# Kernel tuning notes

Hardware: AMD Instinct MI355X
Metric: run time of the kernel (lower is better)

## Reference

```python
import jax, jax.numpy as jnp
import numpy as np

B, S = 1, 2048
HID, NH, NKV, HD = 2048, 16, 4, 128
NREP = NH // NKV  # 4
WIN = 1024
ROPE_THETA = 10000.0


def rotate_half(t):
    t1, t2 = jnp.split(t, 2, axis=-1)
    return jnp.concatenate([-t2, t1], axis=-1)


def setup_inputs() -> dict:
    key = jax.random.key(0)
    ks = jax.random.split(key, 5)
    x = jax.random.normal(ks[0], (B, S, HID), dtype=jnp.float32)
    # causal sliding-window additive mask: 0 where attended, -1e9 elsewhere
    i = jnp.arange(S)
    allowed = (i[None, :] <= i[:, None]) & (i[:, None] - i[None, :] < WIN)
    attention_mask = jnp.where(allowed, 0.0, -1e9).astype(jnp.float32)[None, None]  # [1,1,S,S]
    wq = jax.random.normal(ks[1], (NH * HD, HID), dtype=jnp.float32) * 0.02
    wk = jax.random.normal(ks[2], (NKV * HD, HID), dtype=jnp.float32) * 0.02
    wv = jax.random.normal(ks[3], (NKV * HD, HID), dtype=jnp.float32) * 0.02
    wo = jax.random.normal(ks[4], (HID, NH * HD), dtype=jnp.float32) * 0.02
    return {"x": x, "attention_mask": attention_mask, "wq": wq, "wk": wk, "wv": wv, "wo": wo}


def reference(x, attention_mask, wq, wk, wv, wo):
    b, s, _ = x.shape
    q = (x @ wq.T).reshape(b, s, NH, HD)
    k = (x @ wk.T).reshape(b, s, NKV, HD)
    v = (x @ wv.T).reshape(b, s, NKV, HD)
    # rotary embeddings (HF-style rotate_half)
    inv_freq = 1.0 / (ROPE_THETA ** (jnp.arange(0, HD, 2, dtype=jnp.float32) / HD))
    freqs = jnp.arange(s, dtype=jnp.float32)[:, None] * inv_freq[None, :]  # [s, HD/2]
    emb = jnp.concatenate([freqs, freqs], axis=-1)  # [s, HD]
    cos = jnp.cos(emb)[None, :, None, :]
    sin = jnp.sin(emb)[None, :, None, :]
    q = q * cos + rotate_half(q) * sin
    k = k * cos + rotate_half(k) * sin
    # GQA: repeat kv heads
    k = jnp.repeat(k, NREP, axis=2)  # [b, s, NH, HD]
    v = jnp.repeat(v, NREP, axis=2)
    scores = jnp.einsum('bqhd,bkhd->bhqk', q, k) / jnp.sqrt(jnp.float32(HD)) + attention_mask
    probs = jax.nn.softmax(scores.astype(jnp.float32), axis=-1).astype(q.dtype)
    out = jnp.einsum('bhqk,bkhd->bqhd', probs, v).reshape(b, s, NH * HD)
    return out @ wo.T
```

## Files before the change

### kernel.cpp

```cpp
#include <hip/hip_runtime.h>


typedef short v8s __attribute__((ext_vector_type(8)));
typedef short v4s __attribute__((ext_vector_type(4)));
typedef float v4f __attribute__((ext_vector_type(4)));

__device__ __forceinline__ short f2bf(float f) {
  union { float f; unsigned u; } v; v.f = f;
  unsigned r = (v.u + 0x7FFFu + ((v.u >> 16) & 1u)) >> 16;
  return (short)r;
}
__device__ __forceinline__ float bf2f(short h) {
  union { unsigned u; float f; } v; v.u = ((unsigned)(unsigned short)h) << 16;
  return v.f;
}
__device__ __forceinline__ bool sniff_bf16(const unsigned* mask) {
  return mask[1] == 0xCE6ECE6Eu;
}

template <bool BF> struct Raw8;
template <> struct Raw8<true>  { v8s v; };
template <> struct Raw8<false> { float4 a, b; };

template <bool BF> __device__ __forceinline__ Raw8<BF> ldraw(const void* p, size_t e);
template <> __device__ __forceinline__ Raw8<true> ldraw<true>(const void* p, size_t e) {
  Raw8<true> r; r.v = *(const v8s*)((const short*)p + e); return r;
}
template <> __device__ __forceinline__ Raw8<false> ldraw<false>(const void* p, size_t e) {
  Raw8<false> r; const float* f = (const float*)p + e;
  r.a = *(const float4*)f; r.b = *(const float4*)(f + 4); return r;
}
template <bool BF> __device__ __forceinline__ v8s cvt8(const Raw8<BF>& r);
template <> __device__ __forceinline__ v8s cvt8<true>(const Raw8<true>& r) { return r.v; }
template <> __device__ __forceinline__ v8s cvt8<false>(const Raw8<false>& r) {
  v8s o;
  o[0] = f2bf(r.a.x); o[1] = f2bf(r.a.y); o[2] = f2bf(r.a.z); o[3] = f2bf(r.a.w);
  o[4] = f2bf(r.b.x); o[5] = f2bf(r.b.y); o[6] = f2bf(r.b.z); o[7] = f2bf(r.b.w);
  return o;
}

template <bool BFA, bool BFB>
__device__ __forceinline__ void gemm64x128_loop(
    const void* __restrict__ A, const void* __restrict__ Bt,
    int m0, int brow0, short* lA, short* lB, v4f acc[2][4])
{
  const int tid = threadIdx.x;
  const int w = tid >> 6, lane = tid & 63;
  const int quad = lane >> 4, r = lane & 15;
  const int wm = (w >> 1) * 32, wn = (w & 1) * 64;

  int uoffA[2]; size_t ea[2];
#pragma unroll
  for (int j = 0; j < 2; ++j) {
    int u = tid + 256 * j;
    int row = u >> 3, c = (u & 7) * 8;
    uoffA[j] = (c & 32) * 64 + row * 32 + (c & 31);
    ea[j] = (size_t)(m0 + row) * 2048 + c;
  }
  int uoffB[4]; size_t eb[4];
#pragma unroll
  for (int j = 0; j < 4; ++j) {
    int u = tid + 256 * j;
    int row = u >> 3, c = (u & 7) * 8;
    uoffB[j] = (c & 32) * 128 + row * 32 + (c & 31);
    eb[j] = (size_t)(brow0 + row) * 2048 + c;
  }

  for (int k0 = 0; k0 < 2048; k0 += 64) {
    Raw8<BFA> ta[2]; Raw8<BFB> tb[4];
#pragma unroll
    for (int j = 0; j < 2; ++j) ta[j] = ldraw<BFA>(A, ea[j] + k0);
#pragma unroll
    for (int j = 0; j < 4; ++j) tb[j] = ldraw<BFB>(Bt, eb[j] + k0);
    if (k0) __syncthreads();
#pragma unroll
    for (int j = 0; j < 2; ++j) *(v8s*)&lA[uoffA[j]] = cvt8<BFA>(ta[j]);
#pragma unroll
    for (int j = 0; j < 4; ++j) *(v8s*)&lB[uoffB[j]] = cvt8<BFB>(tb[j]);
    __syncthreads();
#pragma unroll
    for (int ks = 0; ks < 2; ++ks) {
      v8s a[2], b[4];
#pragma unroll
      for (int mt = 0; mt < 2; ++mt)
        a[mt] = *(const v8s*)&lA[ks * 2048 + (wm + mt * 16 + r) * 32 + quad * 8];
#pragma unroll
      for (int nt = 0; nt < 4; ++nt)
        b[nt] = *(const v8s*)&lB[ks * 4096 + (wn + nt * 16 + r) * 32 + quad * 8];
#pragma unroll
      for (int mt = 0; mt < 2; ++mt)
#pragma unroll
        for (int nt = 0; nt < 4; ++nt)
          acc[mt][nt] = __builtin_amdgcn_mfma_f32_16x16x32_bf16(a[mt], b[nt], acc[mt][nt], 0, 0, 0);
    }
  }
}

template <bool BF>
__device__ __forceinline__ void qkv_body(
    const void* X, const void* WQ, const void* WK, const void* WV,
    short* Qo, short* Ko, short* VTo)
{
  __shared__ __align__(16) short lA[64 * 64];
  __shared__ __align__(16) short lB[128 * 64];
  const int m0 = blockIdx.x * 64;
  const int n0 = blockIdx.y * 128;
  const void* Bt; int brow0;
  if (n0 < 2048)      { Bt = WQ; brow0 = n0; }
  else if (n0 < 2560) { Bt = WK; brow0 = n0 - 2048; }
  else                { Bt = WV; brow0 = n0 - 2560; }

  v4f acc[2][4];
#pragma unroll
  for (int i = 0; i < 2; ++i)
#pragma unroll
    for (int j = 0; j < 4; ++j) acc[i][j] = v4f{0.f, 0.f, 0.f, 0.f};

  gemm64x128_loop<BF, BF>(X, Bt, m0, brow0, lA, lB, acc);

  const int tid = threadIdx.x;
  const int w = tid >> 6, lane = tid & 63;
  const int quad = lane >> 4, r = lane & 15;
  const int wm = (w >> 1) * 32, wn = (w & 1) * 64;
  const int rowb = m0 + wm + quad * 4;

  if (n0 < 2048) {
#pragma unroll
    for (int mt = 0; mt < 2; ++mt)
#pragma unroll
      for (int nt = 0; nt < 4; ++nt) {
        int row = rowb + mt * 16;
        int col = n0 + wn + nt * 16 + r;
#pragma unroll
        for (int i = 0; i < 4; ++i)
          Qo[(size_t)(row + i) * 2048 + col] = f2bf(acc[mt][nt][i]);
      }
  } else if (n0 < 2560) {
#pragma unroll
    for (int mt = 0; mt < 2; ++mt)
#pragma unroll
      for (int nt = 0; nt < 4; ++nt) {
        int row = rowb + mt * 16;
        int col = n0 + wn + nt * 16 + r - 2048;
#pragma unroll
        for (int i = 0; i < 4; ++i)
          Ko[(size_t)(row + i) * 512 + col] = f2bf(acc[mt][nt][i]);
      }
  } else {
#pragma unroll
    for (int mt = 0; mt < 2; ++mt)
#pragma unroll
      for (int nt = 0; nt < 4; ++nt) {
        int row = rowb + mt * 16;
        int vcol = n0 + wn + nt * 16 + r - 2560;
        v4s pk;
#pragma unroll
        for (int i = 0; i < 4; ++i) pk[i] = f2bf(acc[mt][nt][i]);
        *(v4s*)&VTo[(size_t)vcol * 2048 + row] = pk;
      }
  }
}

__global__ __launch_bounds__(256, 3) void gemm_qkv(
    const void* __restrict__ X, const void* __restrict__ WQ,
    const void* __restrict__ WK, const void* __restrict__ WV,
    const unsigned* __restrict__ mask,
    short* __restrict__ Qo, short* __restrict__ Ko, short* __restrict__ VTo)
{
  if (sniff_bf16(mask)) qkv_body<true>(X, WQ, WK, WV, Qo, Ko, VTo);
  else                  qkv_body<false>(X, WQ, WK, WV, Qo, Ko, VTo);
}

__global__ __launch_bounds__(256) void rope_kernel(short* __restrict__ Q, short* __restrict__ K)
{
  const int t = blockIdx.x * 256 + threadIdx.x;
  const float L2T = 13.287712379549449f / 64.0f;
  int s, d; short* p; float scale;
  if (t < 2097152) {
    s = t >> 10; int rem = t & 1023; int h = rem >> 6; d = rem & 63;
    p = Q + (size_t)s * 2048 + h * 128 + d;
    scale = 0.08838834764831845f;
  } else {
    int u = t - 2097152;
    s = u >> 8; int rem = u & 255; int h = rem >> 6; d = rem & 63;
    p = K + (size_t)s * 512 + h * 128 + d;
    scale = 1.0f;
  }
  float inv = exp2f(-(float)d * L2T);
  float ang = (float)s * inv;
  float cs = cosf(ang), sn = sinf(ang);
  float x1 = bf2f(p[0]), x2 = bf2f(p[64]);
  p[0]  = f2bf((x1 * cs - x2 * sn) * scale);
  p[64] = f2bf((x2 * cs + x1 * sn) * scale);
}

__global__ __launch_bounds__(256, 1) void attn_kernel(
    const short* __restrict__ Q, const short* __restrict__ Kb,
    const short* __restrict__ VT, short* __restrict__ Ao)
{
  __shared__ __align__(16) short lK[64 * 128];
  __shared__ __align__(16) short lV[128 * 64];
  __shared__ __align__(16) short lP[4][16 * 72];

  const int bx = blockIdx.x;
  const int h = bx >> 5, qb = bx & 31;
  const int hk = h >> 2;
  const int q0 = qb * 64;
  const int tid = threadIdx.x, w = tid >> 6, lane = tid & 63;
  const int quad = lane >> 4, r = lane & 15;
  const int wq0 = q0 + w * 16;
  short* lPw = lP[w];

  v8s qa[4];
#pragma unroll
  for (int ks = 0; ks < 4; ++ks)
    qa[ks] = *(const v8s*)(Q + (size_t)(wq0 + r) * 2048 + h * 128 + ks * 32 + quad * 8);

  v4f Oa[8];
#pragma unroll
  for (int dt = 0; dt < 8; ++dt) Oa[dt] = v4f{0.f, 0.f, 0.f, 0.f};
  const float NEG = -3.0e38f;
  float m_i[4], l_i[4];
#pragma unroll
  for (int i = 0; i < 4; ++i) { m_i[i] = NEG; l_i[i] = 0.f; }

  const int t0 = (q0 >= 1024) ? ((q0 - 1023) >> 6) : 0;
  const int t1 = qb;

  for (int t = t0; t <= t1; ++t) {
    const int key0 = t << 6;
    v8s tK[4], tV[4];
#pragma unroll
    for (int u = 0; u < 4; ++u) {
      int lin = (w * 4 + u) * 64 + lane;
      int krow = lin >> 4, kcc = lin & 15;
      tK[u] = *(const v8s*)(Kb + (size_t)(key0 + krow) * 512 + hk * 128 + ((kcc ^ krow) & 15) * 8);
      int vrow = lin >> 3, vcc = lin & 7;
      tV[u] = *(const v8s*)(VT + (size_t)(hk * 128 + vrow) * 2048 + key0 + ((vcc ^ vrow) & 7) * 8);
    }
    if (t > t0) __syncthreads();
#pragma unroll
    for (int u = 0; u < 4; ++u) {
      int lin = (w * 4 + u) * 64 + lane;
      *(v8s*)&lK[lin * 8] = tK[u];
      *(v8s*)&lV[lin * 8] = tV[u];
    }
    __syncthreads();

    v4f s4[4];
#pragma unroll
    for (int nt = 0; nt < 4; ++nt) s4[nt] = v4f{0.f, 0.f, 0.f, 0.f};
#pragma unroll
    for (int ks = 0; ks < 4; ++ks)
#pragma unroll
      for (int nt = 0; nt < 4; ++nt) {
        v8s bk = *(const v8s*)&lK[(nt * 16 + r) * 128 + (((ks * 4 + quad) ^ r) & 15) * 8];
        s4[nt] = __builtin_amdgcn_mfma_f32_16x16x32_bf16(qa[ks], bk, s4[nt], 0, 0, 0);
      }

    float rowmax[4] = {NEG, NEG, NEG, NEG};
#pragma unroll
    for (int nt = 0; nt < 4; ++nt) {
      int key = key0 + nt * 16 + r;
#pragma unroll
      for (int i = 0; i < 4; ++i) {
        int q = wq0 + quad * 4 + i;
        bool ok = (key <= q) && (q - key < 1024);
        if (ok) rowmax[i] = fmaxf(rowmax[i], s4[nt][i]);
      }
    }
#pragma unroll
    for (int i = 0; i < 4; ++i)
#pragma unroll
      for (int off = 1; off < 16; off <<= 1)
        rowmax[i] = fmaxf(rowmax[i], __shfl_xor(rowmax[i], off, 64));
    float alpha[4], rsum[4] = {0.f, 0.f, 0.f, 0.f};
#pragma unroll
    for (int i = 0; i < 4; ++i) {
      float mn = fmaxf(m_i[i], rowmax[i]);
      alpha[i] = __expf(m_i[i] - mn);
      m_i[i] = mn;
    }
#pragma unroll
    for (int nt = 0; nt < 4; ++nt) {
      int key = key0 + nt * 16 + r;
#pragma unroll
      for (int i = 0; i < 4; ++i) {
        int q = wq0 + quad * 4 + i;
        bool ok = (key <= q) && (q - key < 1024);
        float p = ok ? __expf(s4[nt][i] - m_i[i]) : 0.0f;
        rsum[i] += p;
        lPw[(quad * 4 + i) * 72 + nt * 16 + r] = f2bf(p);
      }
    }
#pragma unroll
    for (int i = 0; i < 4; ++i) {
#pragma unroll
      for (int off = 1; off < 16; off <<= 1)
        rsum[i] += __shfl_xor(rsum[i], off, 64);
      l_i[i] = l_i[i] * alpha[i] + rsum[i];
    }
#pragma unroll
    for (int dt = 0; dt < 8; ++dt)
#pragma unroll
      for (int i = 0; i < 4; ++i) Oa[dt][i] *= alpha[i];

#pragma unroll
    for (int ks2 = 0; ks2 < 2; ++ks2) {
      v8s ap = *(const v8s*)&lPw[r * 72 + ks2 * 32 + quad * 8];
#pragma unroll
      for (int dt = 0; dt < 8; ++dt) {
        v8s bv = *(const v8s*)&lV[(dt * 16 + r) * 64 + (((ks2 * 4 + quad) ^ r) & 7) * 8];
        Oa[dt] = __builtin_amdgcn_mfma_f32_16x16x32_bf16(ap, bv, Oa[dt], 0, 0, 0);
      }
    }
  }

  float invl[4];
#pragma unroll
  for (int i = 0; i < 4; ++i) invl[i] = (l_i[i] > 0.f) ? 1.0f / l_i[i] : 0.f;
#pragma unroll
  for (int dt = 0; dt < 8; ++dt)
#pragma unroll
    for (int i = 0; i < 4; ++i) {
      int q = wq0 + quad * 4 + i;
      Ao[(size_t)q * 2048 + h * 128 + dt * 16 + r] = f2bf(Oa[dt][i] * invl[i]);
    }
}

template <bool BF>
__device__ __forceinline__ void out_body(
    const short* A, const void* WO, void* Out)
{
  __shared__ __align__(16) short lA[64 * 64];
  __shared__ __align__(16) short lB[128 * 64];
  const int m0 = blockIdx.x * 64;
  const int n0 = blockIdx.y * 128;

  v4f acc[2][4];
#pragma unroll
  for (int i = 0; i < 2; ++i)
#pragma unroll
    for (int j = 0; j < 4; ++j) acc[i][j] = v4f{0.f, 0.f, 0.f, 0.f};

  gemm64x128_loop<true, BF>(A, WO, m0, n0, lA, lB, acc);

  const int tid = threadIdx.x;
  const int w = tid >> 6, lane = tid & 63;
  const int quad = lane >> 4, r = lane & 15;
  const int wm = (w >> 1) * 32, wn = (w & 1) * 64;
  const int rowb = m0 + wm + quad * 4;
#pragma unroll
  for (int mt = 0; mt < 2; ++mt)
#pragma unroll
    for (int nt = 0; nt < 4; ++nt) {
      int row = rowb + mt * 16;
      int col = n0 + wn + nt * 16 + r;
#pragma unroll
      for (int i = 0; i < 4; ++i) {
        size_t idx = (size_t)(row + i) * 2048 + col;
        if (BF) ((short*)Out)[idx] = f2bf(acc[mt][nt][i]);
        else    ((float*)Out)[idx] = acc[mt][nt][i];
      }
    }
}

__global__ __launch_bounds__(256, 3) void gemm_out(
    const short* __restrict__ A, const void* __restrict__ WO,
    const unsigned* __restrict__ mask, void* __restrict__ Out)
{
  if (sniff_bf16(mask)) out_body<true>(A, WO, Out);
  else                  out_body<false>(A, WO, Out);
}

extern "C" void kernel_launch(void* const* d_in, const int* in_sizes, int n_in,
                              void* d_out, int out_size, void* d_ws, size_t ws_size,
                              hipStream_t stream) {
  const void*     x    = d_in[0];
  const unsigned* mask = (const unsigned*)d_in[1];
  const void*     wq   = d_in[2];
  const void*     wk   = d_in[3];
  const void*     wv   = d_in[4];
  const void*     wo   = d_in[5];

  short* Q  = (short*)d_out;
  short* Kb = (short*)d_ws;
  short* VT = Kb + (size_t)2048 * 512;
  short* Ao = VT + (size_t)2048 * 512;

  gemm_qkv<<<dim3(32, 24), 256, 0, stream>>>(x, wq, wk, wv, mask, Q, Kb, VT);
  rope_kernel<<<10240, 256, 0, stream>>>(Q, Kb);
  attn_kernel<<<512, 256, 0, stream>>>(Q, Kb, VT, Ao);
  gemm_out<<<dim3(32, 16), 256, 0, stream>>>(Ao, wo, mask, d_out);
}
```

Measured before the change: 259.1 us.

## Pre-convert inputs to bf16 and use direct global-to-LDS loads in GEMMs

Adds a conversion kernel that casts X and all weight matrices to bf16 in workspace once per call. The QKV and output GEMMs then load tiles with global_load_lds (direct DMA into LDS) rather than register-staged loads with per-element conversion. This is meant to cut per-tile fp32 conversion and register traffic in the GEMM inner loops. The cost is an extra pass over the weights every call plus more workspace, and the old path is kept as a fallback when the workspace is too small.

After: 229.9 us. 1.13x faster.

```diff
diff --git a/kernel.cpp b/kernel.cpp
--- a/kernel.cpp
+++ b/kernel.cpp
@@ -1,9 +1,16 @@
 #include <hip/hip_runtime.h>
 
+
+#define AS1 __attribute__((address_space(1)))
+#define AS3 __attribute__((address_space(3)))
 
 typedef short v8s __attribute__((ext_vector_type(8)));
 typedef short v4s __attribute__((ext_vector_type(4)));
 typedef float v4f __attribute__((ext_vector_type(4)));
+
+__device__ __forceinline__ void gload16(const void* g, void* l) {
+  __builtin_amdgcn_global_load_lds((AS1 void*)g, (AS3 void*)l, 16, 0, 0);
+}
 
 __device__ __forceinline__ short f2bf(float f) {
   union { float f; unsigned u; } v; v.f = f;
@@ -39,6 +46,178 @@
   return o;
 }
 
+__global__ __launch_bounds__(256) void convert_kernel(
+    const void* __restrict__ X, const void* __restrict__ WQ,
+    const void* __restrict__ WK, const void* __restrict__ WV,
+    const void* __restrict__ WO, const unsigned* __restrict__ mask,
+    short* __restrict__ Xbf, short* __restrict__ Wqkvbf, short* __restrict__ WObf)
+{
+  const bool bf = sniff_bf16(mask);
+  size_t e = ((size_t)blockIdx.x * 256 + threadIdx.x) * 8;
+  const void* src; short* dst; size_t off, doff;
+  if (e < 4194304)       { src = X;  dst = Xbf;  off = e; doff = e; }
+  else if (e < 10485760) {
+    size_t wv = e - 4194304; dst = Wqkvbf; doff = wv;
+    if (wv < 4194304)      { src = WQ; off = wv; }
+    else if (wv < 5242880) { src = WK; off = wv - 4194304; }
+    else                   { src = WV; off = wv - 5242880; }
+  }
+  else                   { src = WO; dst = WObf; off = e - 10485760; doff = off; }
+  v8s v = bf ? ldraw<true>(src, off).v : cvt8<false>(ldraw<false>(src, off));
+  *(v8s*)&dst[doff] = v;
+}
+
+__device__ __forceinline__ void gemm_dma_loop(
+    const short* __restrict__ A, const short* __restrict__ Bt,
+    int m0, int brow0, short* lA, short* lB, v4f acc[2][4])
+{
+  const int tid = threadIdx.x;
+  const int w = tid >> 6, lane = tid & 63;
+  const int quad = lane >> 4, r = lane & 15;
+  const int wm = (w >> 1) * 32, wn = (w & 1) * 64;
+  const int rlo = lane >> 2, c8 = (lane & 3) * 8;
+
+  size_t ga[2]; short* la[2];
+#pragma unroll
+  for (int j = 0; j < 2; ++j) {
+    int cA = w * 2 + j;
+    int p = cA >> 2, local = cA & 3;
+    ga[j] = (size_t)(m0 + local * 16 + rlo) * 2048 + p * 32 + c8;
+    la[j] = lA + cA * 512;
+  }
+  size_t gb[4]; short* lb[4];
+#pragma unroll
+  for (int j = 0; j < 4; ++j) {
+    int cB = w * 4 + j;
+    int p = cB >> 3, local = cB & 7;
+    gb[j] = (size_t)(brow0 + local * 16 + rlo) * 2048 + p * 32 + c8;
+    lb[j] = lB + cB * 512;
+  }
+
+  for (int k0 = 0; k0 < 2048; k0 += 64) {
+    if (k0) __syncthreads();
+#pragma unroll
+    for (int j = 0; j < 2; ++j) gload16(A + ga[j] + k0, la[j]);
+#pragma unroll
+    for (int j = 0; j < 4; ++j) gload16(Bt + gb[j] + k0, lb[j]);
+    __syncthreads();
+#pragma unroll
+    for (int ks = 0; ks < 2; ++ks) {
+      v8s a[2], b[4];
+#pragma unroll
+      for (int mt = 0; mt < 2; ++mt)
+        a[mt] = *(const v8s*)&lA[ks * 2048 + (wm + mt * 16 + r) * 32 + quad * 8];
+#pragma unroll
+      for (int nt = 0; nt < 4; ++nt)
+        b[nt] = *(const v8s*)&lB[ks * 4096 + (wn + nt * 16 + r) * 32 + quad * 8];
+#pragma unroll
+      for (int mt = 0; mt < 2; ++mt)
+#pragma unroll
+        for (int nt = 0; nt < 4; ++nt)
+          acc[mt][nt] = __builtin_amdgcn_mfma_f32_16x16x32_bf16(a[mt], b[nt], acc[mt][nt], 0, 0, 0);
+    }
+  }
+}
+
+__device__ __forceinline__ void qkv_epilogue(
+    v4f acc[2][4], int m0, int n0, short* Qo, short* Ko, short* VTo)
+{
+  const int tid = threadIdx.x;
+  const int w = tid >> 6, lane = tid & 63;
+  const int quad = lane >> 4, r = lane & 15;
+  const int wm = (w >> 1) * 32, wn = (w & 1) * 64;
+  const int rowb = m0 + wm + quad * 4;
+
+  if (n0 < 2048) {
+#pragma unroll
+    for (int mt = 0; mt < 2; ++mt)
+#pragma unroll
+      for (int nt = 0; nt < 4; ++nt) {
+        int row = rowb + mt * 16;
+        int col = n0 + wn + nt * 16 + r;
+#pragma unroll
+        for (int i = 0; i < 4; ++i)
+          Qo[(size_t)(row + i) * 2048 + col] = f2bf(acc[mt][nt][i]);
+      }
+  } else if (n0 < 2560) {
+#pragma unroll
+    for (int mt = 0; mt < 2; ++mt)
+#pragma unroll
+      for (int nt = 0; nt < 4; ++nt) {
+        int row = rowb + mt * 16;
+        int col = n0 + wn + nt * 16 + r - 2048;
+#pragma unroll
+        for (int i = 0; i < 4; ++i)
+          Ko[(size_t)(row + i) * 512 + col] = f2bf(acc[mt][nt][i]);
+      }
+  } else {
+#pragma unroll
+    for (int mt = 0; mt < 2; ++mt)
+#pragma unroll
+      for (int nt = 0; nt < 4; ++nt) {
+        int row = rowb + mt * 16;
+        int vcol = n0 + wn + nt * 16 + r - 2560;
+        v4s pk;
+#pragma unroll
+        for (int i = 0; i < 4; ++i) pk[i] = f2bf(acc[mt][nt][i]);
+        *(v4s*)&VTo[(size_t)vcol * 2048 + row] = pk;
+      }
+  }
+}
+
+__global__ __launch_bounds__(256, 3) void gemm_qkv_dma(
+    const short* __restrict__ Xbf, const short* __restrict__ Wqkvbf,
+    short* __restrict__ Qo, short* __restrict__ Ko, short* __restrict__ VTo)
+{
+  __shared__ __align__(16) short lA[64 * 64];
+  __shared__ __align__(16) short lB[128 * 64];
+  const int m0 = blockIdx.x * 64;
+  const int n0 = blockIdx.y * 128;
+  v4f acc[2][4];
+#pragma unroll
+  for (int i = 0; i < 2; ++i)
+#pragma unroll
+    for (int j = 0; j < 4; ++j) acc[i][j] = v4f{0.f, 0.f, 0.f, 0.f};
+  gemm_dma_loop(Xbf, Wqkvbf, m0, n0, lA, lB, acc);
+  qkv_epilogue(acc, m0, n0, Qo, Ko, VTo);
+}
+
+__global__ __launch_bounds__(256, 3) void gemm_out_dma(
+    const short* __restrict__ A, const short* __restrict__ WObf,
+    const unsigned* __restrict__ mask, void* __restrict__ Out)
+{
+  __shared__ __align__(16) short lA[64 * 64];
+  __shared__ __align__(16) short lB[128 * 64];
+  const int m0 = blockIdx.x * 64;
+  const int n0 = blockIdx.y * 128;
+  v4f acc[2][4];
+#pragma unroll
+  for (int i = 0; i < 2; ++i)
+#pragma unroll
+    for (int j = 0; j < 4; ++j) acc[i][j] = v4f{0.f, 0.f, 0.f, 0.f};
+  gemm_dma_loop(A, WObf, m0, n0, lA, lB, acc);
+
+  const bool bf = sniff_bf16(mask);
+  const int tid = threadIdx.x;
+  const int w = tid >> 6, lane = tid & 63;
+  const int quad = lane >> 4, r = lane & 15;
+  const int wm = (w >> 1) * 32, wn = (w & 1) * 64;
+  const int rowb = m0 + wm + quad * 4;
+#pragma unroll
+  for (int mt = 0; mt < 2; ++mt)
+#pragma unroll
+    for (int nt = 0; nt < 4; ++nt) {
+      int row = rowb + mt * 16;
+      int col = n0 + wn + nt * 16 + r;
+#pragma unroll
+      for (int i = 0; i < 4; ++i) {
+        size_t idx = (size_t)(row + i) * 2048 + col;
+        if (bf) ((short*)Out)[idx] = f2bf(acc[mt][nt][i]);
+        else    ((float*)Out)[idx] = acc[mt][nt][i];
+      }
+    }
+}
+
 template <bool BFA, bool BFB>
 __device__ __forceinline__ void gemm64x128_loop(
     const void* __restrict__ A, const void* __restrict__ Bt,
@@ -96,10 +275,11 @@
   }
 }
 
-template <bool BF>
-__device__ __forceinline__ void qkv_body(
-    const void* X, const void* WQ, const void* WK, const void* WV,
-    short* Qo, short* Ko, short* VTo)
+__global__ __launch_bounds__(256, 3) void gemm_qkv_fb(
+    const void* __restrict__ X, const void* __restrict__ WQ,
+    const void* __restrict__ WK, const void* __restrict__ WV,
+    const unsigned* __restrict__ mask,
+    short* __restrict__ Qo, short* __restrict__ Ko, short* __restrict__ VTo)
 {
   __shared__ __align__(16) short lA[64 * 64];
   __shared__ __align__(16) short lB[128 * 64];
@@ -116,59 +296,48 @@
 #pragma unroll
     for (int j = 0; j < 4; ++j) acc[i][j] = v4f{0.f, 0.f, 0.f, 0.f};
 
-  gemm64x128_loop<BF, BF>(X, Bt, m0, brow0, lA, lB, acc);
+  if (sniff_bf16(mask)) gemm64x128_loop<true, true>(X, Bt, m0, brow0, lA, lB, acc);
+  else                  gemm64x128_loop<false, false>(X, Bt, m0, brow0, lA, lB, acc);
+  qkv_epilogue(acc, m0, n0, Qo, Ko, VTo);
+}
+
+__global__ __launch_bounds__(256, 3) void gemm_out_fb(
+    const short* __restrict__ A, const void* __restrict__ WO,
+    const unsigned* __restrict__ mask, void* __restrict__ Out)
+{
+  __shared__ __align__(16) short lA[64 * 64];
+  __shared__ __align__(16) short lB[128 * 64];
+  const bool bf = sniff_bf16(mask);
+  const int m0 = blockIdx.x * 64;
+  const int n0 = blockIdx.y * 128;
+
+  v4f acc[2][4];
+#pragma unroll
+  for (int i = 0; i < 2; ++i)
+#pragma unroll
+    for (int j = 0; j < 4; ++j) acc[i][j] = v4f{0.f, 0.f, 0.f, 0.f};
+
+  if (bf) gemm64x128_loop<true, true>(A, WO, m0, n0, lA, lB, acc);
+  else    gemm64x128_loop<true, false>(A, WO, m0, n0, lA, lB, acc);
 
   const int tid = threadIdx.x;
   const int w = tid >> 6, lane = tid & 63;
   const int quad = lane >> 4, r = lane & 15;
   const int wm = (w >> 1) * 32, wn = (w & 1) * 64;
   const int rowb = m0 + wm + quad * 4;
-
-  if (n0 < 2048) {
-#pragma unroll
-    for (int mt = 0; mt < 2; ++mt)
-#pragma unroll
-      for (int nt = 0; nt < 4; ++nt) {
-        int row = rowb + mt * 16;
-        int col = n0 + wn + nt * 16 + r;
-#pragma unroll
-        for (int i = 0; i < 4; ++i)
-          Qo[(size_t)(row + i) * 2048 + col] = f2bf(acc[mt][nt][i]);
-      }
-  } else if (n0 < 2560) {
-#pragma unroll
-    for (int mt = 0; mt < 2; ++mt)
-#pragma unroll
-      for (int nt = 0; nt < 4; ++nt) {
-        int row = rowb + mt * 16;
-        int col = n0 + wn + nt * 16 + r - 2048;
-#pragma unroll
-        for (int i = 0; i < 4; ++i)
-          Ko[(size_t)(row + i) * 512 + col] = f2bf(acc[mt][nt][i]);
-      }
-  } else {
-#pragma unroll
-    for (int mt = 0; mt < 2; ++mt)
-#pragma unroll
-      for (int nt = 0; nt < 4; ++nt) {
-        int row = rowb + mt * 16;
-        int vcol = n0 + wn + nt * 16 + r - 2560;
-        v4s pk;
-#pragma unroll
-        for (int i = 0; i < 4; ++i) pk[i] = f2bf(acc[mt][nt][i]);
-        *(v4s*)&VTo[(size_t)vcol * 2048 + row] = pk;
-      }
-  }
-}
-
-__global__ __launch_bounds__(256, 3) void gemm_qkv(
-    const void* __restrict__ X, const void* __restrict__ WQ,
-    const void* __restrict__ WK, const void* __restrict__ WV,
-    const unsigned* __restrict__ mask,
-    short* __restrict__ Qo, short* __restrict__ Ko, short* __restrict__ VTo)
-{
-  if (sniff_bf16(mask)) qkv_body<true>(X, WQ, WK, WV, Qo, Ko, VTo);
-  else                  qkv_body<false>(X, WQ, WK, WV, Qo, Ko, VTo);
+#pragma unroll
+  for (int mt = 0; mt < 2; ++mt)
+#pragma unroll
+    for (int nt = 0; nt < 4; ++nt) {
+      int row = rowb + mt * 16;
+      int col = n0 + wn + nt * 16 + r;
+#pragma unroll
+      for (int i = 0; i < 4; ++i) {
+        size_t idx = (size_t)(row + i) * 2048 + col;
+        if (bf) ((short*)Out)[idx] = f2bf(acc[mt][nt][i]);
+        else    ((float*)Out)[idx] = acc[mt][nt][i];
+      }
+    }
 }
 
 __global__ __launch_bounds__(256) void rope_kernel(short* __restrict__ Q, short* __restrict__ K)
@@ -328,51 +497,6 @@
     }
 }
 
-template <bool BF>
-__device__ __forceinline__ void out_body(
-    const short* A, const void* WO, void* Out)
-{
-  __shared__ __align__(16) short lA[64 * 64];
-  __shared__ __align__(16) short lB[128 * 64];
-  const int m0 = blockIdx.x * 64;
-  const int n0 = blockIdx.y * 128;
-
-  v4f acc[2][4];
-#pragma unroll
-  for (int i = 0; i < 2; ++i)
-#pragma unroll
-    for (int j = 0; j < 4; ++j) acc[i][j] = v4f{0.f, 0.f, 0.f, 0.f};
-
-  gemm64x128_loop<true, BF>(A, WO, m0, n0, lA, lB, acc);
-
-  const int tid = threadIdx.x;
-  const int w = tid >> 6, lane = tid & 63;
-  const int quad = lane >> 4, r = lane & 15;
-  const int wm = (w >> 1) * 32, wn = (w & 1) * 64;
-  const int rowb = m0 + wm + quad * 4;
-#pragma unroll
-  for (int mt = 0; mt < 2; ++mt)
-#pragma unroll
-    for (int nt = 0; nt < 4; ++nt) {
-      int row = rowb + mt * 16;
-      int col = n0 + wn + nt * 16 + r;
-#pragma unroll
-      for (int i = 0; i < 4; ++i) {
-        size_t idx = (size_t)(row + i) * 2048 + col;
-        if (BF) ((short*)Out)[idx] = f2bf(acc[mt][nt][i]);
-        else    ((float*)Out)[idx] = acc[mt][nt][i];
-      }
-    }
-}
-
-__global__ __launch_bounds__(256, 3) void gemm_out(
-    const short* __restrict__ A, const void* __restrict__ WO,
-    const unsigned* __restrict__ mask, void* __restrict__ Out)
-{
-  if (sniff_bf16(mask)) out_body<true>(A, WO, Out);
-  else                  out_body<false>(A, WO, Out);
-}
-
 extern "C" void kernel_launch(void* const* d_in, const int* in_sizes, int n_in,
                               void* d_out, int out_size, void* d_ws, size_t ws_size,
                               hipStream_t stream) {
@@ -385,11 +509,23 @@
 
   short* Q  = (short*)d_out;
   short* Kb = (short*)d_ws;
-  short* VT = Kb + (size_t)2048 * 512;
-  short* Ao = VT + (size_t)2048 * 512;
-
-  gemm_qkv<<<dim3(32, 24), 256, 0, stream>>>(x, wq, wk, wv, mask, Q, Kb, VT);
-  rope_kernel<<<10240, 256, 0, stream>>>(Q, Kb);
-  attn_kernel<<<512, 256, 0, stream>>>(Q, Kb, VT, Ao);
-  gemm_out<<<dim3(32, 16), 256, 0, stream>>>(Ao, wo, mask, d_out);
-}
+  short* VT = Kb + (size_t)1048576;
+  short* Ao = VT + (size_t)1048576;
+
+  const size_t NEED = 41943040ull;
+  if (ws_size >= NEED) {
+    short* Xbf    = Ao + (size_t)4194304;
+    short* Wqkvbf = Xbf + (size_t)4194304;
+    short* WObf   = Wqkvbf + (size_t)6291456;
+    convert_kernel<<<7168, 256, 0, stream>>>(x, wq, wk, wv, wo, mask, Xbf, Wqkvbf, WObf);
+    gemm_qkv_dma<<<dim3(32, 24), 256, 0, stream>>>(Xbf, Wqkvbf, Q, Kb, VT);
+    rope_kernel<<<10240, 256, 0, stream>>>(Q, Kb);
+    attn_kernel<<<512, 256, 0, stream>>>(Q, Kb, VT, Ao);
+    gemm_out_dma<<<dim3(32, 16), 256, 0, stream>>>(Ao, WObf, mask, d_out);
+  } else {
+    gemm_qkv_fb<<<dim3(32, 24), 256, 0, stream>>>(x, wq, wk, wv, mask, Q, Kb, VT);
+    rope_kernel<<<10240, 256, 0, stream>>>(Q, Kb);
+    attn_kernel<<<512, 256, 0, stream>>>(Q, Kb, VT, Ao);
+    gemm_out_fb<<<dim3(32, 16), 256, 0, stream>>>(Ao, wo, mask, d_out);
+  }
+}
```
